# Performance work log

Hardware: AMD Instinct MI355X
Metric: run time of the kernel (lower is better)

Reference implementation:

```python
import jax, jax.numpy as jnp
import numpy as np

H, N, BSZ, L = 512, 64, 8, 2048
DT_MIN, DT_MAX = 1e-3, 1e-1


def _hippo_dplr(n_state):
    """HiPPO-LegS -> DPLR (Lambda, P, B) init, as in the Annotated S4."""
    n = np.arange(n_state, dtype=np.float64)
    p = np.sqrt(n + 0.5)                      # low-rank factor P
    pm = np.sqrt(1.0 + 2.0 * n)
    A = np.tril(pm[:, None] * pm[None, :]) - np.diag(n)
    A = -A                                    # HiPPO-LegS A
    S = A + p[:, None] * p[None, :]           # normal part (skew-symmetric + cI)
    lam_real = np.mean(np.diagonal(S)) * np.ones(n_state)
    lam_imag, V = np.linalg.eigh(S * -1j)
    Lam = lam_real + 1j * lam_imag
    B = np.sqrt(2.0 * n + 1.0)
    return Lam, V.conj().T @ p, V.conj().T @ B


def setup_inputs() -> dict:
    key = jax.random.key(0)
    k1, k2, k3, k4, k5 = jax.random.split(key, 5)
    Lam, P, B = _hippo_dplr(N)
    return {
        "u": jax.random.normal(k1, (BSZ, L, H), dtype=jnp.float32),
        "Lambda_real": jnp.asarray(Lam.real, jnp.float32),
        "Lambda_imag": jnp.asarray(Lam.imag, jnp.float32),
        "P_real": jnp.asarray(P.real, jnp.float32),
        "P_imag": jnp.asarray(P.imag, jnp.float32),
        "B_real": jnp.asarray(B.real, jnp.float32),
        "B_imag": jnp.asarray(B.imag, jnp.float32),
        "C_real": jax.random.normal(k2, (H, N), jnp.float32) * 0.5,
        "C_imag": jax.random.normal(k3, (H, N), jnp.float32) * 0.5,
        "log_dt": jax.random.uniform(k4, (H,), jnp.float32,
                                     float(np.log(DT_MIN)), float(np.log(DT_MAX))),
        "D": jax.random.normal(k5, (H,), jnp.float32) * 0.01,
    }


def _s4_forward(u, Lr, Li, Pr, Pi, Br, Bi, Cr, Ci, log_dt, D):
    Lam = (Lr + 1j * Li).astype(jnp.complex64)   # (N,)
    P = (Pr + 1j * Pi).astype(jnp.complex64)     # (N,)
    B = (Br + 1j * Bi).astype(jnp.complex64)     # (N,)
    C = (Cr + 1j * Ci).astype(jnp.complex64)     # (H, N)
    l_len = u.shape[1]
    dt = jnp.exp(log_dt)                         # (H,)

    # --- DPLR kernel via Cauchy-kernel generating function (bilinear disc),
    # batched over all H channels instead of the per-channel Python loop. ---
    omega = jnp.exp(-2j * jnp.pi * jnp.arange(l_len, dtype=jnp.float32) / l_len)
    omega = omega.astype(jnp.complex64)          # roots of unity, (L,)
    g = (2.0 / dt)[:, None].astype(jnp.complex64) * ((1.0 - omega) / (1.0 + omega))[None, :]  # (H, L)
    c2 = 2.0 / (1.0 + omega)                     # (L,)
    r = 1.0 / (g[:, :, None] - Lam[None, None, :])  # Cauchy resolvent (H, L, N)
    Cc = jnp.conj(C)                             # (H, N)
    Qc = jnp.conj(P)                             # (N,)
    k00 = jnp.einsum('hn,hln->hl', Cc * B[None, :], r)
    k01 = jnp.einsum('hn,hln->hl', Cc * P[None, :], r)
    k10 = jnp.einsum('n,hln->hl', Qc * B, r)
    k11 = jnp.einsum('n,hln->hl', Qc * P, r)
    at_roots = c2[None, :] * (k00 - k01 * k10 / (1.0 + k11))  # (H, L)
    K = jnp.fft.ifft(at_roots, axis=-1).real.astype(u.dtype)  # (H, L) conv kernel

    # --- causal FFT convolution per channel ---
    x = jnp.swapaxes(u, -1, -2)                  # (B, H, L)
    n_fft = 2 * l_len
    Xf = jnp.fft.rfft(x, n=n_fft)
    Kf = jnp.fft.rfft(K, n=n_fft)
    y = jnp.fft.irfft(Xf * Kf[None], n=n_fft)[..., :l_len]
    y = y + x * D[None, :, None]                 # skip connection
    return jnp.swapaxes(y, -1, -2)               # (B, L, H)


def reference(u, Lambda_real, Lambda_imag, P_real, P_imag, B_real, B_imag,
              C_real, C_imag, log_dt, D):
    return _s4_forward(u, Lambda_real, Lambda_imag, P_real, P_imag,
                       B_real, B_imag, C_real, C_imag, log_dt, D)
```

## Files before the change

### kernel.cpp

```cpp
#include <hip/hip_runtime.h>
#include <math.h>

#define LSEQ 2048
#define HCH  512
#define NST  64
#define NBATCH 8
#define PIf 3.14159265358979f

#define PHYS(i) ((i) + ((i) >> 3))
#define LDSN 2304

__device__ __forceinline__ float2 cmul(float2 a, float2 b) {
    return make_float2(a.x * b.x - a.y * b.y, a.x * b.y + a.y * b.x);
}
__device__ __forceinline__ float2 cadd(float2 a, float2 b) { return make_float2(a.x + b.x, a.y + b.y); }
__device__ __forceinline__ float2 csub(float2 a, float2 b) { return make_float2(a.x - b.x, a.y - b.y); }
__device__ __forceinline__ float2 csq(float2 a) { return make_float2(a.x * a.x - a.y * a.y, 2.f * a.x * a.y); }
template<int INV>
__device__ __forceinline__ float2 rot90(float2 a) {
    return INV ? make_float2(-a.y, a.x) : make_float2(a.y, -a.x);
}

template<int INV, int STAGE>
__device__ __forceinline__ void radix8_pass(const float2* __restrict__ src,
                                            float2* __restrict__ dst, int tid)
{
    const int Ns  = 1 << STAGE;
    const int lam = tid & (Ns - 1);
    const int G   = ((tid >> STAGE) << (STAGE + 3)) + lam;

    float2 x0 = src[PHYS(tid)];
    float2 x1 = src[PHYS(tid + 256)];
    float2 x2 = src[PHYS(tid + 512)];
    float2 x3 = src[PHYS(tid + 768)];
    float2 x4 = src[PHYS(tid + 1024)];
    float2 x5 = src[PHYS(tid + 1280)];
    float2 x6 = src[PHYS(tid + 1536)];
    float2 x7 = src[PHYS(tid + 1792)];

    const float SGN = INV ? 1.f : -1.f;
    float sn, cs;
    __sincosf(SGN * (PIf / (float)(4 * Ns)) * (float)lam, &sn, &cs);
    const float2 T3 = make_float2(cs, sn);
    const float2 T2 = csq(T3);
    const float2 T1 = csq(T2);
    const float r2 = 0.70710678118f;
    const float2 U = cmul(T3, make_float2(r2, SGN * r2));

    float2 t;
    t = cmul(T1, x4); float2 a0 = cadd(x0, t), a4 = csub(x0, t);
    t = cmul(T1, x5); float2 a1 = cadd(x1, t), a5 = csub(x1, t);
    t = cmul(T1, x6); float2 a2 = cadd(x2, t), a6 = csub(x2, t);
    t = cmul(T1, x7); float2 a3 = cadd(x3, t), a7 = csub(x3, t);
    t = cmul(T2, a2);             float2 b0 = cadd(a0, t), b2 = csub(a0, t);
    t = cmul(T2, a3);             float2 b1 = cadd(a1, t), b3 = csub(a1, t);
    t = rot90<INV>(cmul(T2, a6)); float2 b4 = cadd(a4, t), b6 = csub(a4, t);
    t = rot90<INV>(cmul(T2, a7)); float2 b5 = cadd(a5, t), b7 = csub(a5, t);
    t = cmul(T3, b1);             dst[PHYS(G)]          = cadd(b0, t); dst[PHYS(G + 4 * Ns)] = csub(b0, t);
    t = rot90<INV>(cmul(T3, b3)); dst[PHYS(G + 2 * Ns)] = cadd(b2, t); dst[PHYS(G + 6 * Ns)] = csub(b2, t);
    t = cmul(U, b5);              dst[PHYS(G + Ns)]     = cadd(b4, t); dst[PHYS(G + 5 * Ns)] = csub(b4, t);
    t = rot90<INV>(cmul(U, b7));  dst[PHYS(G + 3 * Ns)] = cadd(b6, t); dst[PHYS(G + 7 * Ns)] = csub(b6, t);
}

template<int INV>
__device__ float2* fft2048(float2* bufA, float2* bufB)
{
    const int tid = threadIdx.x;
    __syncthreads();
    radix8_pass<INV, 0>(bufA, bufB, tid);
    __syncthreads();
    radix8_pass<INV, 3>(bufB, bufA, tid);
    __syncthreads();
    radix8_pass<INV, 6>(bufA, bufB, tid);
    __syncthreads();
    const float SGN = INV ? 1.f : -1.f;
#pragma unroll
    for (int q = 0; q < 2; ++q) {
        const int j = tid + (q << 8);
        float2 A  = bufB[PHYS(j)];
        float2 C  = bufB[PHYS(j + 512)];
        float2 B  = bufB[PHYS(j + 1024)];
        float2 Dd = bufB[PHYS(j + 1536)];
        float sn, cs;
        __sincosf(SGN * (PIf / 1024.f) * (float)j, &sn, &cs);
        const float2 v = make_float2(cs, sn);
        const float2 w = csq(v);
        float2 t = cmul(w, B);  float2 m1 = cadd(A, t), m2 = csub(A, t);
        t = cmul(w, Dd);        float2 m3 = cadd(C, t), m4 = csub(C, t);
        const float2 t3 = cmul(v, m3);
        const float2 t4 = rot90<INV>(cmul(v, m4));
        bufA[PHYS(j)]        = cadd(m1, t3);
        bufA[PHYS(j + 1024)] = csub(m1, t3);
        bufA[PHYS(j + 512)]  = cadd(m2, t4);
        bufA[PHYS(j + 1536)] = csub(m2, t4);
    }
    __syncthreads();
    return bufA;
}

template<int INV, int STAGE>
__device__ __forceinline__ void radix8_inplace(float2* __restrict__ buf, int tid)
{
    __syncthreads();
    float2 x0 = buf[PHYS(tid)];
    float2 x1 = buf[PHYS(tid + 256)];
    float2 x2 = buf[PHYS(tid + 512)];
    float2 x3 = buf[PHYS(tid + 768)];
    float2 x4 = buf[PHYS(tid + 1024)];
    float2 x5 = buf[PHYS(tid + 1280)];
    float2 x6 = buf[PHYS(tid + 1536)];
    float2 x7 = buf[PHYS(tid + 1792)];
    __syncthreads();

    const int Ns  = 1 << STAGE;
    const int lam = tid & (Ns - 1);
    const int G   = ((tid >> STAGE) << (STAGE + 3)) + lam;
    const float SGN = INV ? 1.f : -1.f;
    float sn, cs;
    __sincosf(SGN * (PIf / (float)(4 * Ns)) * (float)lam, &sn, &cs);
    const float2 T3 = make_float2(cs, sn);
    const float2 T2 = csq(T3);
    const float2 T1 = csq(T2);
    const float r2 = 0.70710678118f;
    const float2 U = cmul(T3, make_float2(r2, SGN * r2));
    float2 t;
    t = cmul(T1, x4); float2 a0 = cadd(x0, t), a4 = csub(x0, t);
    t = cmul(T1, x5); float2 a1 = cadd(x1, t), a5 = csub(x1, t);
    t = cmul(T1, x6); float2 a2 = cadd(x2, t), a6 = csub(x2, t);
    t = cmul(T1, x7); float2 a3 = cadd(x3, t), a7 = csub(x3, t);
    t = cmul(T2, a2);             float2 b0 = cadd(a0, t), b2 = csub(a0, t);
    t = cmul(T2, a3);             float2 b1 = cadd(a1, t), b3 = csub(a1, t);
    t = rot90<INV>(cmul(T2, a6)); float2 b4 = cadd(a4, t), b6 = csub(a4, t);
    t = rot90<INV>(cmul(T2, a7)); float2 b5 = cadd(a5, t), b7 = csub(a5, t);
    t = cmul(T3, b1);             buf[PHYS(G)]          = cadd(b0, t); buf[PHYS(G + 4 * Ns)] = csub(b0, t);
    t = rot90<INV>(cmul(T3, b3)); buf[PHYS(G + 2 * Ns)] = cadd(b2, t); buf[PHYS(G + 6 * Ns)] = csub(b2, t);
    t = cmul(U, b5);              buf[PHYS(G + Ns)]     = cadd(b4, t); buf[PHYS(G + 5 * Ns)] = csub(b4, t);
    t = rot90<INV>(cmul(U, b7));  buf[PHYS(G + 3 * Ns)] = cadd(b6, t); buf[PHYS(G + 7 * Ns)] = csub(b6, t);
}

template<int INV>
__device__ __forceinline__ void radix4_inplace(float2* __restrict__ buf, int tid)
{
    __syncthreads();
    const float SGN = INV ? 1.f : -1.f;
#pragma unroll
    for (int q = 0; q < 2; ++q) {
        const int j = tid + (q << 8);
        float2 A  = buf[PHYS(j)];
        float2 C  = buf[PHYS(j + 512)];
        float2 B  = buf[PHYS(j + 1024)];
        float2 Dd = buf[PHYS(j + 1536)];
        float sn, cs;
        __sincosf(SGN * (PIf / 1024.f) * (float)j, &sn, &cs);
        const float2 v = make_float2(cs, sn);
        const float2 w = csq(v);
        float2 t = cmul(w, B);  float2 m1 = cadd(A, t), m2 = csub(A, t);
        t = cmul(w, Dd);        float2 m3 = cadd(C, t), m4 = csub(C, t);
        const float2 t3 = cmul(v, m3);
        const float2 t4 = rot90<INV>(cmul(v, m4));
        buf[PHYS(j)]        = cadd(m1, t3);
        buf[PHYS(j + 1024)] = csub(m1, t3);
        buf[PHYS(j + 512)]  = cadd(m2, t4);
        buf[PHYS(j + 1536)] = csub(m2, t4);
    }
}

template<int INV>
__device__ __forceinline__ void fft2048_ip(float2* buf, int tid)
{
    radix8_inplace<INV, 0>(buf, tid);
    radix8_inplace<INV, 3>(buf, tid);
    radix8_inplace<INV, 6>(buf, tid);
    radix4_inplace<INV>(buf, tid);
}

__global__ __launch_bounds__(256, 4)
void s4_cauchy_kernel(const float* __restrict__ Lr, const float* __restrict__ Li,
                      const float* __restrict__ Pr, const float* __restrict__ Pi,
                      const float* __restrict__ Br, const float* __restrict__ Bi,
                      const float* __restrict__ Cr, const float* __restrict__ Ci,
                      const float* __restrict__ log_dt, float2* __restrict__ at_out)
{
    __shared__ float4 F0[NST];
    __shared__ float4 F1[NST];
    __shared__ float  q1s[NST];

    const int h    = blockIdx.x >> 1;
    const int half = blockIdx.x & 1;
    const int tid  = threadIdx.x;

    if (tid < NST) {
        const float pr = Pr[tid], pi = Pi[tid], br = Br[tid], bi = Bi[tid];
        const float cr = Cr[h * NST + tid], ci = Ci[h * NST + tid];
        F0[tid]  = make_float4(Lr[tid], Li[tid], cr * br + ci * bi, cr * bi - ci * br);
        F1[tid]  = make_float4(cr * pr + ci * pi, cr * pi - ci * pr,
                               pr * br + pi * bi, pr * bi - pi * br);
        q1s[tid] = pr * pr + pi * pi;
    }
    __syncthreads();

    const float dt = expf(log_dt[h]);
    const float a  = 2.0f / dt;

    float tt[4], g[4];
#pragma unroll
    for (int p = 0; p < 4; ++p) {
        const int l = (half << 10) + (p << 8) + tid;
        tt[p] = tanf(PIf * (float)l * (1.0f / 2048.0f));
        g[p]  = a * tt[p];
    }

    float k00r[4], k00i[4], k01r[4], k01i[4];
    float k10r[4], k10i[4], k11r[4], k11i[4];
#pragma unroll
    for (int p = 0; p < 4; ++p) {
        k00r[p] = 0.f; k00i[p] = 0.f; k01r[p] = 0.f; k01i[p] = 0.f;
        k10r[p] = 0.f; k10i[p] = 0.f; k11r[p] = 0.f; k11i[p] = 0.f;
    }

#pragma unroll 2
    for (int n = 0; n < NST; ++n) {
        const float4 f0 = F0[n];
        const float4 f1 = F1[n];
        const float q1 = q1s[n];
        const float x  = -f0.x;
        const float x2 = x * x;
#pragma unroll
        for (int p = 0; p < 4; ++p) {
            const float y   = g[p] - f0.y;
            const float inv = __builtin_amdgcn_rcpf(fmaf(y, y, x2));
            const float rr  = x * inv;
            const float ri  = -y * inv;
            k00r[p] = fmaf(f0.z, rr, fmaf(-f0.w, ri, k00r[p]));
            k00i[p] = fmaf(f0.z, ri, fmaf( f0.w, rr, k00i[p]));
            k01r[p] = fmaf(f1.x, rr, fmaf(-f1.y, ri, k01r[p]));
            k01i[p] = fmaf(f1.x, ri, fmaf( f1.y, rr, k01i[p]));
            k10r[p] = fmaf(f1.z, rr, fmaf(-f1.w, ri, k10r[p]));
            k10i[p] = fmaf(f1.z, ri, fmaf( f1.w, rr, k10i[p]));
            k11r[p] = fmaf(q1, rr, k11r[p]);
            k11i[p] = fmaf(q1, ri, k11i[p]);
        }
    }

    float2* __restrict__ row = at_out + (size_t)h * 2048;
#pragma unroll
    for (int p = 0; p < 4; ++p) {
        const int l = (half << 10) + (p << 8) + tid;
        const float dr = 1.0f + k11r[p], di = k11i[p];
        const float dinv = __builtin_amdgcn_rcpf(fmaf(dr, dr, di * di));
        const float pr_ = k01r[p] * k10r[p] - k01i[p] * k10i[p];
        const float pi_ = k01r[p] * k10i[p] + k01i[p] * k10r[p];
        const float qr = (pr_ * dr + pi_ * di) * dinv;
        const float qi = (pi_ * dr - pr_ * di) * dinv;
        const float sr = k00r[p] - qr, si = k00i[p] - qi;
        row[l] = make_float2(fmaf(-tt[p], si, sr), fmaf(tt[p], sr, si));
    }
}

__global__ __launch_bounds__(256, 4)
void s4_kf_kernel(const float2* __restrict__ at_in, float2* __restrict__ Kf)
{
    __shared__ float2 bufA[LDSN];
    __shared__ float2 bufB[LDSN];

    const int h   = blockIdx.x;
    const int tid = threadIdx.x;
    const float2* __restrict__ at = at_in + (size_t)h * 2048;

    for (int q = 0; q < 8; ++q) {
        const int l = tid + (q << 8);
        bufA[PHYS(l)] = at[l];
    }

    float2* Kt = fft2048<1>(bufA, bufB);

    const float sc = 1.0f / 2048.0f;
    for (int n = tid; n < 1024; n += 256)
        bufB[PHYS(n)] = make_float2(Kt[PHYS(2 * n)].x * sc, Kt[PHYS(2 * n + 1)].x * sc);
    for (int n = 1024 + tid; n < 2048; n += 256)
        bufB[PHYS(n)] = make_float2(0.f, 0.f);

    float2* Z = fft2048<0>(bufB, bufA);

    float2* __restrict__ out = Kf + (size_t)h * 2049;
    for (int k = tid; k < 1024; k += 256) {
        const float2 Zk = Z[PHYS(k)];
        const float2 Zm = Z[PHYS((2048 - k) & 2047)];
        const float zer = 0.5f * (Zk.x + Zm.x), zei = 0.5f * (Zk.y - Zm.y);
        const float zdr = Zk.x - Zm.x,         zdi = Zk.y + Zm.y;
        const float zor = 0.5f * zdi,          zoi = -0.5f * zdr;
        float s, c;
        __sincosf(-PIf * (float)k * (1.0f / 2048.0f), &s, &c);
        const float txr = c * zor - s * zoi;
        const float txi = c * zoi + s * zor;
        out[k] = make_float2(zer + txr, zei + txi);
        if (k > 0) {
            out[2048 - k] = make_float2(zer - txr, txi - zei);
        } else {
            out[2048] = make_float2(Zk.x - Zk.y, 0.f);
        }
    }
    if (tid == 0) {
        const float2 z = Z[PHYS(1024)];
        out[1024] = make_float2(z.x, -z.y);
    }
}

__global__ __launch_bounds__(256, 6)
void s4_conv_kernel(const float* __restrict__ u, float* ws_rows,
                    const float2* __restrict__ Kf, const float* __restrict__ Dv,
                    float* __restrict__ out, int fastpath)
{
    __shared__ float2 buf[LDSN];

    const int bh  = blockIdx.x;
    const int b   = bh >> 9;
    const int h   = bh & 511;
    const int tid = threadIdx.x;

    if (fastpath) {
        const float2* rowv = (const float2*)(ws_rows + (size_t)bh * LSEQ);
        for (int n = tid; n < 1024; n += 256) buf[PHYS(n)] = rowv[n];
    } else {
        const float* ub = u + (size_t)b * LSEQ * HCH + h;
        for (int n = tid; n < 1024; n += 256)
            buf[PHYS(n)] = make_float2(ub[(size_t)(2 * n) * HCH],
                                       ub[(size_t)(2 * n + 1) * HCH]);
    }
    for (int n = 1024 + tid; n < 2048; n += 256) buf[PHYS(n)] = make_float2(0.f, 0.f);

    fft2048_ip<0>(buf, tid);

    const float2* __restrict__ kf = Kf + (size_t)h * 2049;

    __syncthreads();
    float2 Zk[4], Zm[4], Z1024v;
#pragma unroll
    for (int q = 0; q < 4; ++q) {
        const int k = tid + (q << 8);
        Zk[q] = buf[PHYS(k)];
        Zm[q] = buf[PHYS((2048 - k) & 2047)];
    }
    if (tid == 0) Z1024v = buf[PHYS(1024)];
    __syncthreads();

#pragma unroll
    for (int q = 0; q < 4; ++q) {
        const int k = tid + (q << 8);
        const float2 zk = Zk[q], zm = Zm[q];
        const float zer = 0.5f * (zk.x + zm.x), zei = 0.5f * (zk.y - zm.y);
        const float zdr = zk.x - zm.x,          zdi = zk.y + zm.y;
        const float zor = 0.5f * zdi,           zoi = -0.5f * zdr;
        float s, c;
        __sincosf(-PIf * (float)k * (1.0f / 2048.0f), &s, &c);
        const float txr = c * zor - s * zoi;
        const float txi = c * zoi + s * zor;
        const float2 Xk = make_float2(zer + txr, zei + txi);
        float2 Yk = cmul(Xk, kf[k]);
        float2 Ym;
        if (k > 0) {
            const float2 Xm = make_float2(zer - txr, txi - zei);
            Ym = cmul(Xm, kf[2048 - k]);
        } else {
            const float x2048 = zk.x - zk.y;
            const float2 k2 = kf[2048];
            Ym = make_float2(x2048 * k2.x, x2048 * k2.y);
        }
        const float yer = 0.5f * (Yk.x + Ym.x), yei = 0.5f * (Yk.y - Ym.y);
        const float ydr = Yk.x - Ym.x,          ydi = Yk.y + Ym.y;
        const float yor = 0.5f * (c * ydr + s * ydi);
        const float yoi = 0.5f * (c * ydi - s * ydr);
        buf[PHYS(k)] = make_float2(yer - yoi, yei + yor);
        if (k > 0)
            buf[PHYS(2048 - k)] = make_float2(yer + yoi, yor - yei);
    }
    if (tid == 0) {
        const float2 kk = kf[1024];
        const float2 y = make_float2(Z1024v.x * kk.x + Z1024v.y * kk.y,
                                     Z1024v.x * kk.y - Z1024v.y * kk.x);
        buf[PHYS(1024)] = make_float2(y.x, -y.y);
    }

    fft2048_ip<1>(buf, tid);

    __syncthreads();
    const float Dh = Dv[h];
    const float sc = 1.0f / 2048.0f;
    if (fastpath) {
        float2* rowv = (float2*)(ws_rows + (size_t)bh * LSEQ);
        for (int n = tid; n < 1024; n += 256) {
            const float2 wv = buf[PHYS(n)];
            const float2 xv = rowv[n];
            rowv[n] = make_float2(wv.x * sc + Dh * xv.x,
                                  wv.y * sc + Dh * xv.y);
        }
    } else {
        const float* ub = u + (size_t)b * LSEQ * HCH + h;
        float* ob = out + (size_t)b * LSEQ * HCH + h;
        for (int n = tid; n < 1024; n += 256) {
            const float2 wv = buf[PHYS(n)];
            ob[(size_t)(2 * n) * HCH]     = wv.x * sc + Dh * ub[(size_t)(2 * n) * HCH];
            ob[(size_t)(2 * n + 1) * HCH] = wv.y * sc + Dh * ub[(size_t)(2 * n + 1) * HCH];
        }
    }
}

__global__ __launch_bounds__(256)
void transpose_kernel(const float* __restrict__ in, float* __restrict__ out,
                      int rows, int cols)
{
    __shared__ float tile[32][33];
    const int b  = blockIdx.z;
    const int r0 = blockIdx.y << 5;
    const int c0 = blockIdx.x << 5;
    const size_t base = (size_t)b * rows * cols;
    const int tx = threadIdx.x & 31;
    const int ty = threadIdx.x >> 5;
#pragma unroll
    for (int i = 0; i < 32; i += 8)
        tile[ty + i][tx] = in[base + (size_t)(r0 + ty + i) * cols + (c0 + tx)];
    __syncthreads();
#pragma unroll
    for (int i = 0; i < 32; i += 8)
        out[base + (size_t)(c0 + ty + i) * rows + (r0 + tx)] = tile[tx][ty + i];
}

extern "C" void kernel_launch(void* const* d_in, const int* in_sizes, int n_in,
                              void* d_out, int out_size, void* d_ws, size_t ws_size,
                              hipStream_t stream)
{
    (void)in_sizes; (void)n_in; (void)out_size;
    const float* u  = (const float*)d_in[0];
    const float* Lr = (const float*)d_in[1];
    const float* Li = (const float*)d_in[2];
    const float* Pr = (const float*)d_in[3];
    const float* Pi = (const float*)d_in[4];
    const float* Br = (const float*)d_in[5];
    const float* Bi = (const float*)d_in[6];
    const float* Cr = (const float*)d_in[7];
    const float* Ci = (const float*)d_in[8];
    const float* ld = (const float*)d_in[9];
    const float* Dv = (const float*)d_in[10];
    float* out = (float*)d_out;

    const size_t UT_BYTES = (size_t)NBATCH * HCH * LSEQ * sizeof(float);
    const size_t KF_BYTES = (size_t)HCH * 2049 * sizeof(float2);
    const int fast = (ws_size >= UT_BYTES + KF_BYTES) ? 1 : 0;

    float*  ut;
    float2* Kf;
    if (fast) { ut = (float*)d_ws; Kf = (float2*)((char*)d_ws + UT_BYTES); }
    else      { ut = (float*)d_ws; Kf = (float2*)d_ws; }

    float2* at = (float2*)d_out;

    hipLaunchKernelGGL(s4_cauchy_kernel, dim3(HCH * 2), dim3(256), 0, stream,
                       Lr, Li, Pr, Pi, Br, Bi, Cr, Ci, ld, at);
    hipLaunchKernelGGL(s4_kf_kernel, dim3(HCH), dim3(256), 0, stream, at, Kf);
    if (fast) {
        hipLaunchKernelGGL(transpose_kernel, dim3(HCH / 32, LSEQ / 32, NBATCH),
                           dim3(256), 0, stream, u, ut, LSEQ, HCH);
    }
    hipLaunchKernelGGL(s4_conv_kernel, dim3(NBATCH * HCH), dim3(256), 0, stream,
                       u, fast ? ut : nullptr, Kf, Dv, out, fast);
    if (fast) {
        hipLaunchKernelGGL(transpose_kernel, dim3(LSEQ / 32, HCH / 32, NBATCH),
                           dim3(256), 0, stream, ut, out, HCH, LSEQ);
    }
}
```

Before: 109.7 us.

## Drop transpose kernels and read input strided directly in conv kernel

Removes the two transpose kernels and the workspace-staged row path, so the convolution kernel always loads and stores the (B,L,H) tensors with stride H. This avoids the extra round trips through global memory for the transposed copies and two kernel launches. In exchange, each wavefront issues uncoalesced strided accesses and relies on L2 sharing across neighbouring channel blocks. Occupancy is also raised by tightening launch bounds to 8 blocks per CU.

```diff
diff --git a/kernel.cpp b/kernel.cpp
--- a/kernel.cpp
+++ b/kernel.cpp
@@ -306,10 +306,9 @@
     }
 }
 
-__global__ __launch_bounds__(256, 6)
-void s4_conv_kernel(const float* __restrict__ u, float* ws_rows,
-                    const float2* __restrict__ Kf, const float* __restrict__ Dv,
-                    float* __restrict__ out, int fastpath)
+__global__ __launch_bounds__(256, 8)
+void s4_conv_kernel(const float* __restrict__ u, const float2* __restrict__ Kf,
+                    const float* __restrict__ Dv, float* __restrict__ out)
 {
     __shared__ float2 buf[LDSN];
 
@@ -318,15 +317,11 @@
     const int h   = bh & 511;
     const int tid = threadIdx.x;
 
-    if (fastpath) {
-        const float2* rowv = (const float2*)(ws_rows + (size_t)bh * LSEQ);
-        for (int n = tid; n < 1024; n += 256) buf[PHYS(n)] = rowv[n];
-    } else {
-        const float* ub = u + (size_t)b * LSEQ * HCH + h;
-        for (int n = tid; n < 1024; n += 256)
-            buf[PHYS(n)] = make_float2(ub[(size_t)(2 * n) * HCH],
-                                       ub[(size_t)(2 * n + 1) * HCH]);
-    }
+    const float* __restrict__ ub = u + (size_t)b * LSEQ * HCH + h;
+
+    for (int n = tid; n < 1024; n += 256)
+        buf[PHYS(n)] = make_float2(ub[(size_t)(2 * n) * HCH],
+                                   ub[(size_t)(2 * n + 1) * HCH]);
     for (int n = 1024 + tid; n < 2048; n += 256) buf[PHYS(n)] = make_float2(0.f, 0.f);
 
     fft2048_ip<0>(buf, tid);
@@ -386,50 +381,19 @@
     __syncthreads();
     const float Dh = Dv[h];
     const float sc = 1.0f / 2048.0f;
-    if (fastpath) {
-        float2* rowv = (float2*)(ws_rows + (size_t)bh * LSEQ);
-        for (int n = tid; n < 1024; n += 256) {
-            const float2 wv = buf[PHYS(n)];
-            const float2 xv = rowv[n];
-            rowv[n] = make_float2(wv.x * sc + Dh * xv.x,
-                                  wv.y * sc + Dh * xv.y);
-        }
-    } else {
-        const float* ub = u + (size_t)b * LSEQ * HCH + h;
-        float* ob = out + (size_t)b * LSEQ * HCH + h;
-        for (int n = tid; n < 1024; n += 256) {
-            const float2 wv = buf[PHYS(n)];
-            ob[(size_t)(2 * n) * HCH]     = wv.x * sc + Dh * ub[(size_t)(2 * n) * HCH];
-            ob[(size_t)(2 * n + 1) * HCH] = wv.y * sc + Dh * ub[(size_t)(2 * n + 1) * HCH];
-        }
-    }
-}
-
-__global__ __launch_bounds__(256)
-void transpose_kernel(const float* __restrict__ in, float* __restrict__ out,
-                      int rows, int cols)
-{
-    __shared__ float tile[32][33];
-    const int b  = blockIdx.z;
-    const int r0 = blockIdx.y << 5;
-    const int c0 = blockIdx.x << 5;
-    const size_t base = (size_t)b * rows * cols;
-    const int tx = threadIdx.x & 31;
-    const int ty = threadIdx.x >> 5;
-#pragma unroll
-    for (int i = 0; i < 32; i += 8)
-        tile[ty + i][tx] = in[base + (size_t)(r0 + ty + i) * cols + (c0 + tx)];
-    __syncthreads();
-#pragma unroll
-    for (int i = 0; i < 32; i += 8)
-        out[base + (size_t)(c0 + ty + i) * rows + (r0 + tx)] = tile[tx][ty + i];
+    float* __restrict__ ob = out + (size_t)b * LSEQ * HCH + h;
+    for (int n = tid; n < 1024; n += 256) {
+        const float2 wv = buf[PHYS(n)];
+        ob[(size_t)(2 * n) * HCH]     = wv.x * sc + Dh * ub[(size_t)(2 * n) * HCH];
+        ob[(size_t)(2 * n + 1) * HCH] = wv.y * sc + Dh * ub[(size_t)(2 * n + 1) * HCH];
+    }
 }
 
 extern "C" void kernel_launch(void* const* d_in, const int* in_sizes, int n_in,
                               void* d_out, int out_size, void* d_ws, size_t ws_size,
                               hipStream_t stream)
 {
-    (void)in_sizes; (void)n_in; (void)out_size;
+    (void)in_sizes; (void)n_in; (void)out_size; (void)ws_size;
     const float* u  = (const float*)d_in[0];
     const float* Lr = (const float*)d_in[1];
     const float* Li = (const float*)d_in[2];
@@ -443,28 +407,12 @@
     const float* Dv = (const float*)d_in[10];
     float* out = (float*)d_out;
 
-    const size_t UT_BYTES = (size_t)NBATCH * HCH * LSEQ * sizeof(float);
-    const size_t KF_BYTES = (size_t)HCH * 2049 * sizeof(float2);
-    const int fast = (ws_size >= UT_BYTES + KF_BYTES) ? 1 : 0;
-
-    float*  ut;
-    float2* Kf;
-    if (fast) { ut = (float*)d_ws; Kf = (float2*)((char*)d_ws + UT_BYTES); }
-    else      { ut = (float*)d_ws; Kf = (float2*)d_ws; }
-
+    float2* Kf = (float2*)d_ws;
     float2* at = (float2*)d_out;
 
     hipLaunchKernelGGL(s4_cauchy_kernel, dim3(HCH * 2), dim3(256), 0, stream,
                        Lr, Li, Pr, Pi, Br, Bi, Cr, Ci, ld, at);
     hipLaunchKernelGGL(s4_kf_kernel, dim3(HCH), dim3(256), 0, stream, at, Kf);
-    if (fast) {
-        hipLaunchKernelGGL(transpose_kernel, dim3(HCH / 32, LSEQ / 32, NBATCH),
-                           dim3(256), 0, stream, u, ut, LSEQ, HCH);
-    }
     hipLaunchKernelGGL(s4_conv_kernel, dim3(NBATCH * HCH), dim3(256), 0, stream,
-                       u, fast ? ut : nullptr, Kf, Dv, out, fast);
-    if (fast) {
-        hipLaunchKernelGGL(transpose_kernel, dim3(LSEQ / 32, HCH / 32, NBATCH),
-                           dim3(256), 0, stream, ut, out, HCH, LSEQ);
-    }
-}
+                       u, Kf, Dv, out);
+}
```

Result: slower. 303.3 us (+176.6%).
